# Kernel tuning notes

Measured on AMD Instinct MI355X. Metric: run time of the kernel, lower is better.

Reference implementation:

```python
import jax, jax.numpy as jnp
import numpy as np

DIM = 384
NUM_HEADS = 6
HEAD_DIM = DIM // NUM_HEADS
MLP_HIDDEN = 4 * DIM
SCALE = HEAD_DIM ** -0.5
EPS = 1e-5


def layer_norm(x, w, b):
    mu = jnp.mean(x, axis=-1, keepdims=True)
    var = jnp.mean(jnp.square(x - mu), axis=-1, keepdims=True)
    return (x - mu) * jax.lax.rsqrt(var + EPS) * w + b


def setup_inputs() -> dict:
    key = jax.random.key(0)
    ks = jax.random.split(key, 24)
    d = DIM
    s = 0.02
    inp = {
        'x1': jax.random.normal(ks[0], (16, d, 32, 32), jnp.float32),
        'x2': jax.random.normal(ks[1], (16, d, 32, 32), jnp.float32),
        # per-branch attention-input LayerNorm + kqv projection (no bias)
        'ln_a1_w': jnp.ones((d,), jnp.float32), 'ln_a1_b': jnp.zeros((d,), jnp.float32),
        'kqv1_w': jax.random.normal(ks[2], (d, 3 * d), jnp.float32) * s,
        'ln_a2_w': jnp.ones((d,), jnp.float32), 'ln_a2_b': jnp.zeros((d,), jnp.float32),
        'kqv2_w': jax.random.normal(ks[3], (d, 3 * d), jnp.float32) * s,
        # output projections
        'proj1_w': jax.random.normal(ks[4], (d, d), jnp.float32) * s,
        'proj1_b': jnp.zeros((d,), jnp.float32),
        'proj2_w': jax.random.normal(ks[5], (d, d), jnp.float32) * s,
        'proj2_b': jnp.zeros((d,), jnp.float32),
        # post-attention LayerNorms
        'ln1_w': jnp.ones((d,), jnp.float32), 'ln1_b': jnp.zeros((d,), jnp.float32),
        'ln2_w': jnp.ones((d,), jnp.float32), 'ln2_b': jnp.zeros((d,), jnp.float32),
        # MLPs
        'mlp1_fc1_w': jax.random.normal(ks[6], (d, MLP_HIDDEN), jnp.float32) * s,
        'mlp1_fc1_b': jnp.zeros((MLP_HIDDEN,), jnp.float32),
        'mlp1_fc2_w': jax.random.normal(ks[7], (MLP_HIDDEN, d), jnp.float32) * s,
        'mlp1_fc2_b': jnp.zeros((d,), jnp.float32),
        'mlp2_fc1_w': jax.random.normal(ks[8], (d, MLP_HIDDEN), jnp.float32) * s,
        'mlp2_fc1_b': jnp.zeros((MLP_HIDDEN,), jnp.float32),
        'mlp2_fc2_w': jax.random.normal(ks[9], (MLP_HIDDEN, d), jnp.float32) * s,
        'mlp2_fc2_b': jnp.zeros((d,), jnp.float32),
    }
    return inp


def _kqv_branch(x, ln_w, ln_b, Wkqv):
    # x: [B, C, H, W] -> embedding [B, N, C]; k,q,v: [B, h, N, hd]
    B, C, H, W = x.shape
    N = H * W
    emb = x.reshape(B, C, N).transpose(0, 2, 1)
    xn = layer_norm(emb, ln_w, ln_b)
    kqv = (xn @ Wkqv).reshape(B, N, 3, NUM_HEADS, HEAD_DIM).transpose(2, 0, 3, 1, 4)
    return kqv[0], kqv[1], kqv[2], emb


def _cross_attn(q, k, v):
    # q,k,v: [B, h, N, hd] -> [B, N, C]
    scores = jnp.einsum('bhnd,bhmd->bhnm', q, k) * SCALE
    a = jax.nn.softmax(scores, axis=-1)
    o = jnp.einsum('bhnm,bhmd->bhnd', a, v)
    B, h, N, hd = o.shape
    return o.transpose(0, 2, 1, 3).reshape(B, N, h * hd)


def reference(x1, x2, ln_a1_w, ln_a1_b, kqv1_w, ln_a2_w, ln_a2_b, kqv2_w,
              proj1_w, proj1_b, proj2_w, proj2_b, ln1_w, ln1_b, ln2_w, ln2_b,
              mlp1_fc1_w, mlp1_fc1_b, mlp1_fc2_w, mlp1_fc2_b,
              mlp2_fc1_w, mlp2_fc1_b, mlp2_fc2_w, mlp2_fc2_b):
    B, C, H, W = x1.shape
    k1, q1, v1, emb1 = _kqv_branch(x1, ln_a1_w, ln_a1_b, kqv1_w)
    k2, q2, v2, emb2 = _kqv_branch(x2, ln_a2_w, ln_a2_b, kqv2_w)
    a1 = _cross_attn(q1, k2, v2)   # branch 1 queries attend to branch 2
    a2 = _cross_attn(q2, k1, v1)
    out1 = emb1 + (a1 @ proj1_w + proj1_b)
    h1 = layer_norm(out1, ln1_w, ln1_b)
    out1 = out1 + (jax.nn.gelu(h1 @ mlp1_fc1_w + mlp1_fc1_b, approximate=False) @ mlp1_fc2_w + mlp1_fc2_b)
    out2 = emb2 + (a2 @ proj2_w + proj2_b)
    h2 = layer_norm(out2, ln2_w, ln2_b)
    out2 = out2 + (jax.nn.gelu(h2 @ mlp2_fc1_w + mlp2_fc1_b, approximate=False) @ mlp2_fc2_w + mlp2_fc2_b)
    out1 = out1.transpose(0, 2, 1).reshape(B, C, H, W)
    out2 = out2.transpose(0, 2, 1).reshape(B, C, H, W)
    return (out1, out2)
```

## Files before the change

### kernel.cpp

```cpp
#include <hip/hip_runtime.h>
#include <math.h>

typedef unsigned short u16;
typedef __attribute__((ext_vector_type(8))) short short8;
typedef __attribute__((ext_vector_type(4))) float f32x4;

#define MFMA(a,b,c) __builtin_amdgcn_mfma_f32_16x16x32_bf16(a, b, c, 0, 0, 0)
#define SWZ(row, ch) ((((ch) ^ ((row) & 7)) << 3))
#define EXP2F(x) __builtin_amdgcn_exp2f(x)

__device__ __forceinline__ float b2f(u16 v) {
    union { unsigned int i; float f; } c; c.i = ((unsigned int)v) << 16; return c.f;
}
__device__ __forceinline__ u16 f2b(float f) {
    union { float f; unsigned int i; } c; c.f = f;
    unsigned int u = c.i;
    return (u16)((u + 0x7fffu + ((u >> 16) & 1u)) >> 16);
}
__device__ __forceinline__ u16 f2b_p(float f) {
    union { float f; unsigned int i; } c; c.f = f;
    return (u16)((c.i + 0x8000u) >> 16);
}

struct TWArgs { const float* src[8]; u16* dst[8]; int K[8]; int N[8]; };

__global__ __launch_bounds__(256) void transpose_w(TWArgs a) {
    int wi = blockIdx.z;
    int K = a.K[wi], N = a.N[wi];
    int n0 = blockIdx.x * 32, k0 = blockIdx.y * 32;
    if (n0 >= N || k0 >= K) return;
    __shared__ float t[32][33];
    const float* s = a.src[wi]; u16* d = a.dst[wi];
    int tx = threadIdx.x & 31, ty = threadIdx.x >> 5;
    for (int i = 0; i < 32; i += 8)
        t[ty + i][tx] = s[(size_t)(k0 + ty + i) * N + n0 + tx];
    __syncthreads();
    for (int i = 0; i < 32; i += 8)
        d[(size_t)(n0 + ty + i) * K + k0 + tx] = f2b(t[tx][ty + i]);
}

__global__ __launch_bounds__(256)
void ln_tr(const float* __restrict__ x0, const float* __restrict__ x1,
           const float* __restrict__ w0, const float* __restrict__ bb0,
           const float* __restrict__ w1, const float* __restrict__ bb1,
           u16* __restrict__ xn0, u16* __restrict__ xn1) {
    int br = blockIdx.z;
    const float* x  = br ? x1 : x0;
    const float* wv = br ? w1 : w0;
    const float* bv = br ? bb1 : bb0;
    u16* xn = br ? xn1 : xn0;
    int b = blockIdx.y, n0 = blockIdx.x * 32;
    __shared__ float tile[32][385];
    __shared__ float smu[32], srs[32];
    int tid = threadIdx.x;
    const float* xb = x + (size_t)b * 384 * 1024 + n0;
    for (int idx = tid; idx < 384 * 32; idx += 256) {
        int c = idx >> 5, nn = idx & 31;
        tile[nn][c] = xb[(size_t)c * 1024 + nn];
    }
    __syncthreads();
    {
        int nn = tid >> 3, part = tid & 7;
        float s1 = 0.f, s2 = 0.f;
        for (int c = part * 48; c < part * 48 + 48; ++c) {
            float v = tile[nn][c]; s1 += v; s2 += v * v;
        }
        for (int off = 1; off < 8; off <<= 1) {
            s1 += __shfl_xor(s1, off, 64); s2 += __shfl_xor(s2, off, 64);
        }
        if (part == 0) {
            float mu = s1 * (1.f / 384.f);
            float var = s2 * (1.f / 384.f) - mu * mu;
            smu[nn] = mu; srs[nn] = rsqrtf(fmaxf(var, 0.f) + 1e-5f);
        }
    }
    __syncthreads();
    size_t rowbase = (size_t)b * 1024 + n0;
    for (int idx = tid; idx < 32 * 384; idx += 256) {
        int nn = idx / 384, c = idx - nn * 384;
        float v = tile[nn][c];
        float g = (v - smu[nn]) * srs[nn] * wv[c] + bv[c];
        xn[(rowbase + nn) * 384 + c] = f2b(g);
    }
}

__global__ __launch_bounds__(256)
void ln_rows(const float* __restrict__ i0, const float* __restrict__ i1,
             const float* __restrict__ w0, const float* __restrict__ bb0,
             const float* __restrict__ w1, const float* __restrict__ bb1,
             u16* __restrict__ o0, u16* __restrict__ o1) {
    int br = blockIdx.z;
    const float* in = br ? i1 : i0;
    const float* wv = br ? w1 : w0;
    const float* bv = br ? bb1 : bb0;
    u16* out = br ? o1 : o0;
    int w = threadIdx.x >> 6, l = threadIdx.x & 63;
    size_t row = (size_t)blockIdx.x * 4 + w;
    const float* p = in + row * 384;
    float v[6]; float s1 = 0.f, s2 = 0.f;
    #pragma unroll
    for (int j = 0; j < 6; j++) { v[j] = p[j * 64 + l]; s1 += v[j]; s2 += v[j] * v[j]; }
    for (int off = 1; off < 64; off <<= 1) {
        s1 += __shfl_xor(s1, off, 64); s2 += __shfl_xor(s2, off, 64);
    }
    float mu = s1 * (1.f / 384.f);
    float var = s2 * (1.f / 384.f) - mu * mu;
    float rs = rsqrtf(fmaxf(var, 0.f) + 1e-5f);
    #pragma unroll
    for (int j = 0; j < 6; j++) {
        int c = j * 64 + l;
        out[row * 384 + c] = f2b((v[j] - mu) * rs * wv[c] + bv[c]);
    }
}

template <int EPI>
__global__ __launch_bounds__(256)
void gemm128(const u16* __restrict__ A0, const u16* __restrict__ A1,
             const u16* __restrict__ B0, const u16* __restrict__ B1,
             void* C0v, void* C1v,
             const float* __restrict__ bias0, const float* __restrict__ bias1,
             const void* R0v, const void* R1v,
             int N, int K) {
    const int br = blockIdx.z;
    const u16* A = br ? A1 : A0;
    const u16* B = br ? B1 : B0;
    void* Cv = br ? C1v : C0v;
    const float* bias = br ? bias1 : bias0;
    const void* Rv = br ? R1v : R0v;

    const int n0 = blockIdx.x * 128;
    const int m0 = blockIdx.y * 128;
    const int tid = threadIdx.x;
    const int w = tid >> 6, l = tid & 63;
    const int wm = w >> 1, wn = w & 1;
    const int lr = l & 15, lq = l >> 4;

    __shared__ alignas(16) u16 As[2][128 * 40];
    __shared__ alignas(16) u16 Bs[2][128 * 40];

    f32x4 acc[4][4];
    #pragma unroll
    for (int i = 0; i < 4; i++)
        #pragma unroll
        for (int j = 0; j < 4; j++) acc[i][j] = (f32x4)0.0f;

    const int ar0 = tid >> 2, ac0 = (tid & 3) * 8;
    const int ar1 = ar0 + 64;
    const u16* Ap0 = A + (size_t)(m0 + ar0) * K + ac0;
    const u16* Ap1 = A + (size_t)(m0 + ar1) * K + ac0;
    const u16* Bp0 = B + (size_t)(n0 + ar0) * K + ac0;
    const u16* Bp1 = B + (size_t)(n0 + ar1) * K + ac0;

    const int nk = K >> 5;
    uint4 pa0 = *(const uint4*)Ap0, pa1 = *(const uint4*)Ap1;
    uint4 pb0 = *(const uint4*)Bp0, pb1 = *(const uint4*)Bp1;
    *(uint4*)&As[0][ar0 * 40 + ac0] = pa0;
    *(uint4*)&As[0][ar1 * 40 + ac0] = pa1;
    *(uint4*)&Bs[0][ar0 * 40 + ac0] = pb0;
    *(uint4*)&Bs[0][ar1 * 40 + ac0] = pb1;
    pa0 = *(const uint4*)(Ap0 + 32); pa1 = *(const uint4*)(Ap1 + 32);
    pb0 = *(const uint4*)(Bp0 + 32); pb1 = *(const uint4*)(Bp1 + 32);
    __syncthreads();

    for (int kt = 0; kt < nk; ++kt) {
        const int cur = kt & 1;
        if (kt + 1 < nk) {
            const int nx = cur ^ 1;
            *(uint4*)&As[nx][ar0 * 40 + ac0] = pa0;
            *(uint4*)&As[nx][ar1 * 40 + ac0] = pa1;
            *(uint4*)&Bs[nx][ar0 * 40 + ac0] = pb0;
            *(uint4*)&Bs[nx][ar1 * 40 + ac0] = pb1;
        }
        if (kt + 2 < nk) {
            const int kb = (kt + 2) * 32;
            pa0 = *(const uint4*)(Ap0 + kb); pa1 = *(const uint4*)(Ap1 + kb);
            pb0 = *(const uint4*)(Bp0 + kb); pb1 = *(const uint4*)(Bp1 + kb);
        }
        short8 af[4], bf[4];
        #pragma unroll
        for (int mt = 0; mt < 4; ++mt)
            af[mt] = *(const short8*)&As[cur][(wm * 64 + mt * 16 + lr) * 40 + lq * 8];
        #pragma unroll
        for (int nt = 0; nt < 4; ++nt)
            bf[nt] = *(const short8*)&Bs[cur][(wn * 64 + nt * 16 + lr) * 40 + lq * 8];
        #pragma unroll
        for (int mt = 0; mt < 4; ++mt)
            #pragma unroll
            for (int nt = 0; nt < 4; ++nt)
                acc[mt][nt] = MFMA(af[mt], bf[nt], acc[mt][nt]);
        __syncthreads();
    }

    #pragma unroll
    for (int mt = 0; mt < 4; ++mt)
        #pragma unroll
        for (int nt = 0; nt < 4; ++nt) {
            const int col = n0 + wn * 64 + nt * 16 + lr;
            const int rbase = m0 + wm * 64 + mt * 16 + lq * 4;
            const float bv = (EPI == 0) ? 0.f : bias[col];
            #pragma unroll
            for (int r = 0; r < 4; r++) {
                const int row = rbase + r;
                const size_t idx = (size_t)row * N + col;
                float v = acc[mt][nt][r];
                if (EPI == 0) {
                    if (col < 768) {
                        ((u16*)Cv)[idx] = f2b(col >= 384 ? v * 0.18033688f : v);
                    } else {
                        u16* vtb = (u16*)Rv;
                        vtb[((((size_t)(row >> 10)) * 6 + ((col - 768) >> 6)) * 64
                             + (col & 63)) * 1024 + (row & 1023)] = f2b(v);
                    }
                } else if (EPI == 1) {
                    float xr = ((const float*)Rv)[
                        ((size_t)(row >> 10) * 384 + col) * 1024 + (row & 1023)];
                    ((float*)Cv)[idx] = v + bv + xr;
                } else if (EPI == 2) {
                    v += bv;
                    float g = 0.5f * v * (1.f + erff(v * 0.70710678118f));
                    ((u16*)Cv)[idx] = f2b(g);
                } else {
                    ((float*)Cv)[idx] = v + bv + ((const float*)Rv)[idx];
                }
            }
        }
}

__global__ __launch_bounds__(256)
void attn_k(const u16* __restrict__ kqvA, const u16* __restrict__ kqvB,
            const u16* __restrict__ vtA, const u16* __restrict__ vtB,
            u16* __restrict__ oA, u16* __restrict__ oB) {
    const int bid = blockIdx.x;
    const int g = bid & 7, qb = (bid >> 3) & 7, s = bid >> 6;
    const int grp = s * 8 + g;
    const int ob = grp & 1, h = (grp >> 1) % 6, b = grp / 12;

    const u16* kqvQ  = (ob ? kqvB : kqvA) + (size_t)b * 1024 * 1152;
    const u16* kqvKV = (ob ? kqvA : kqvB) + (size_t)b * 1024 * 1152;
    const u16* vt    = (ob ? vtA : vtB) + ((size_t)b * 6 + h) * 64 * 1024;
    u16* outp = (ob ? oB : oA) + (size_t)b * 1024 * 384;
    const u16* qp = kqvQ + 384 + h * 64;
    const u16* kp = kqvKV + h * 64;

    __shared__ alignas(16) u16 Ks[64 * 64];
    __shared__ alignas(16) u16 Vts[64 * 64];
    __shared__ alignas(16) u16 Ps[4 * 32 * 64];

    const int tid = threadIdx.x, w = tid >> 6, l = tid & 63;
    const int lr = l & 15, lq = l >> 4;
    u16* Psw = Ps + w * 32 * 64;

    short8 qf[2][2];
    #pragma unroll
    for (int a = 0; a < 2; a++)
        #pragma unroll
        for (int ks = 0; ks < 2; ks++)
            qf[a][ks] = *(const short8*)&qp[
                (size_t)(qb * 128 + w * 32 + a * 16 + lr) * 1152 + ks * 32 + lq * 8];

    const int srow = tid >> 3, sch = tid & 7;
    uint4 kpre[2][2], vpre[2][2];
    #pragma unroll
    for (int t = 0; t < 2; t++)
        #pragma unroll
        for (int i = 0; i < 2; i++) {
            int row = srow + i * 32;
            kpre[t][i] = *(const uint4*)&kp[(size_t)(t * 64 + row) * 1152 + sch * 8];
            vpre[t][i] = *(const uint4*)&vt[(size_t)row * 1024 + t * 64 + sch * 8];
        }

    f32x4 oacc[2][4];
    float psum[2][4];
    #pragma unroll
    for (int a = 0; a < 2; a++)
        #pragma unroll
        for (int n = 0; n < 4; n++) oacc[a][n] = (f32x4)0.0f;
    #pragma unroll
    for (int a = 0; a < 2; a++)
        #pragma unroll
        for (int r = 0; r < 4; r++) psum[a][r] = 0.f;

    for (int jt = 0; jt < 16; ++jt) {
        const int slot = jt & 1;
        #pragma unroll
        for (int i = 0; i < 2; i++) {
            int row = srow + i * 32;
            int o = row * 64 + SWZ(row, sch);
            *(uint4*)&Ks[o] = kpre[slot][i];
            *(uint4*)&Vts[o] = vpre[slot][i];
        }
        __syncthreads();
        if (jt + 2 < 16) {
            #pragma unroll
            for (int i = 0; i < 2; i++) {
                int row = srow + i * 32;
                kpre[slot][i] = *(const uint4*)&kp[(size_t)((jt + 2) * 64 + row) * 1152 + sch * 8];
                vpre[slot][i] = *(const uint4*)&vt[(size_t)row * 1024 + (jt + 2) * 64 + sch * 8];
            }
        }

        f32x4 sacc[2][4];
        #pragma unroll
        for (int a = 0; a < 2; a++)
            #pragma unroll
            for (int n = 0; n < 4; n++) sacc[a][n] = (f32x4)0.0f;
        #pragma unroll
        for (int ks = 0; ks < 2; ++ks) {
            short8 bk[4];
            #pragma unroll
            for (int n = 0; n < 4; n++) {
                int row = n * 16 + lr;
                bk[n] = *(const short8*)&Ks[row * 64 + SWZ(row, ks * 4 + lq)];
            }
            #pragma unroll
            for (int a = 0; a < 2; a++)
                #pragma unroll
                for (int n = 0; n < 4; n++) sacc[a][n] = MFMA(qf[a][ks], bk[n], sacc[a][n]);
        }

        #pragma unroll
        for (int a = 0; a < 2; a++)
            #pragma unroll
            for (int r = 0; r < 4; r++) {
                int prow = a * 16 + lq * 4 + r;
                float ps = 0.f;
                #pragma unroll
                for (int n = 0; n < 4; n++) {
                    float p = EXP2F(sacc[a][n][r]);
                    ps += p;
                    Psw[prow * 64 + ((((2 * n + (lr >> 3)) ^ (prow & 7)) << 3) + (lr & 7))] = f2b_p(p);
                }
                psum[a][r] += ps;
            }

        #pragma unroll
        for (int ks = 0; ks < 2; ++ks) {
            short8 ap[2], bv4[4];
            #pragma unroll
            for (int a = 0; a < 2; a++) {
                int row = a * 16 + lr;
                ap[a] = *(const short8*)&Psw[row * 64 + SWZ(row, ks * 4 + lq)];
            }
            #pragma unroll
            for (int n = 0; n < 4; n++) {
                int row = n * 16 + lr;
                bv4[n] = *(const short8*)&Vts[row * 64 + SWZ(row, ks * 4 + lq)];
            }
            #pragma unroll
            for (int a = 0; a < 2; a++)
                #pragma unroll
                for (int n = 0; n < 4; n++) oacc[a][n] = MFMA(ap[a], bv4[n], oacc[a][n]);
        }
        __syncthreads();
    }

    #pragma unroll
    for (int a = 0; a < 2; a++)
        #pragma unroll
        for (int r = 0; r < 4; r++) {
            float sm = psum[a][r];
            sm += __shfl_xor(sm, 1, 64); sm += __shfl_xor(sm, 2, 64);
            sm += __shfl_xor(sm, 4, 64); sm += __shfl_xor(sm, 8, 64);
            psum[a][r] = 1.f / sm;
        }
    #pragma unroll
    for (int a = 0; a < 2; a++)
        #pragma unroll
        for (int n = 0; n < 4; n++)
            #pragma unroll
            for (int r = 0; r < 4; r++) {
                size_t row = (size_t)qb * 128 + w * 32 + a * 16 + lq * 4 + r;
                int col = h * 64 + n * 16 + lr;
                outp[row * 384 + col] = f2b(oacc[a][n][r] * psum[a][r]);
            }
}

__global__ __launch_bounds__(256)
void transpose_out(const float* __restrict__ r0, const float* __restrict__ r1,
                   float* __restrict__ out) {
    int z = blockIdx.z, ob = z >> 4, b = z & 15;
    const float* rp = ob ? r1 : r0;
    int c0 = blockIdx.y * 32, n0 = blockIdx.x * 32;
    __shared__ float t[32][33];
    int tx = threadIdx.x & 31, ty = threadIdx.x >> 5;
    for (int i = 0; i < 32; i += 8)
        t[ty + i][tx] = rp[((size_t)b * 1024 + n0 + ty + i) * 384 + c0 + tx];
    __syncthreads();
    for (int i = 0; i < 32; i += 8)
        out[(size_t)ob * 6291456 + ((size_t)b * 384 + c0 + ty + i) * 1024 + n0 + tx]
            = t[tx][ty + i];
}

extern "C" void kernel_launch(void* const* d_in, const int* in_sizes, int n_in,
                              void* d_out, int out_size, void* d_ws, size_t ws_size,
                              hipStream_t stream) {
    const float* x1      = (const float*)d_in[0];
    const float* x2      = (const float*)d_in[1];
    const float* ln_a1_w = (const float*)d_in[2];
    const float* ln_a1_b = (const float*)d_in[3];
    const float* kqv1_w  = (const float*)d_in[4];
    const float* ln_a2_w = (const float*)d_in[5];
    const float* ln_a2_b = (const float*)d_in[6];
    const float* kqv2_w  = (const float*)d_in[7];
    const float* proj1_w = (const float*)d_in[8];
    const float* proj1_b = (const float*)d_in[9];
    const float* proj2_w = (const float*)d_in[10];
    const float* proj2_b = (const float*)d_in[11];
    const float* ln1_w   = (const float*)d_in[12];
    const float* ln1_b   = (const float*)d_in[13];
    const float* ln2_w   = (const float*)d_in[14];
    const float* ln2_b   = (const float*)d_in[15];
    const float* m1f1w   = (const float*)d_in[16];
    const float* m1f1b   = (const float*)d_in[17];
    const float* m1f2w   = (const float*)d_in[18];
    const float* m1f2b   = (const float*)d_in[19];
    const float* m2f1w   = (const float*)d_in[20];
    const float* m2f1b   = (const float*)d_in[21];
    const float* m2f2w   = (const float*)d_in[22];
    const float* m2f2b   = (const float*)d_in[23];
    (void)in_sizes; (void)n_in; (void)out_size; (void)ws_size;

    const size_t R = 16384;
    char* ws = (char*)d_ws;
    size_t off = 0;
    auto alloc = [&](size_t bytes) -> char* {
        char* p = ws + off;
        off = (off + bytes + 255) & ~(size_t)255;
        return p;
    };
    u16* kqv1t  = (u16*)alloc(1152 * 384 * 2);
    u16* kqv2t  = (u16*)alloc(1152 * 384 * 2);
    u16* proj1t = (u16*)alloc(384 * 384 * 2);
    u16* proj2t = (u16*)alloc(384 * 384 * 2);
    u16* fc11t  = (u16*)alloc(1536 * 384 * 2);
    u16* fc12t  = (u16*)alloc(1536 * 384 * 2);
    u16* fc21t  = (u16*)alloc(384 * 1536 * 2);
    u16* fc22t  = (u16*)alloc(384 * 1536 * 2);
    u16* xn1 = (u16*)alloc(R * 384 * 2);
    u16* xn2 = (u16*)alloc(R * 384 * 2);
    char* regC = alloc(R * 1152 * 2 * 2);
    u16* kqv1 = (u16*)regC;
    u16* kqv2 = (u16*)(regC + R * 1152 * 2);
    float* oa1 = (float*)regC;
    float* oa2 = (float*)(regC + R * 384 * 4);
    u16* hid_b2 = (u16*)(regC + 2 * R * 384 * 4);
    u16* at1 = (u16*)d_out;
    u16* at2 = at1 + R * 384;
    u16* vt1 = at2 + R * 384;
    u16* vt2 = vt1 + (size_t)16 * 6 * 64 * 1024;
    u16* hid_b1 = (u16*)d_out;

    TWArgs tw;
    tw.src[0] = kqv1_w;  tw.dst[0] = kqv1t;  tw.K[0] = 384;  tw.N[0] = 1152;
    tw.src[1] = kqv2_w;  tw.dst[1] = kqv2t;  tw.K[1] = 384;  tw.N[1] = 1152;
    tw.src[2] = proj1_w; tw.dst[2] = proj1t; tw.K[2] = 384;  tw.N[2] = 384;
    tw.src[3] = proj2_w; tw.dst[3] = proj2t; tw.K[3] = 384;  tw.N[3] = 384;
    tw.src[4] = m1f1w;   tw.dst[4] = fc11t;  tw.K[4] = 384;  tw.N[4] = 1536;
    tw.src[5] = m2f1w;   tw.dst[5] = fc12t;  tw.K[5] = 384;  tw.N[5] = 1536;
    tw.src[6] = m1f2w;   tw.dst[6] = fc21t;  tw.K[6] = 1536; tw.N[6] = 384;
    tw.src[7] = m2f2w;   tw.dst[7] = fc22t;  tw.K[7] = 1536; tw.N[7] = 384;
    transpose_w<<<dim3(48, 48, 8), dim3(256), 0, stream>>>(tw);

    ln_tr<<<dim3(32, 16, 2), dim3(256), 0, stream>>>(
        x1, x2, ln_a1_w, ln_a1_b, ln_a2_w, ln_a2_b, xn1, xn2);

    gemm128<0><<<dim3(9, 128, 2), dim3(256), 0, stream>>>(
        xn1, xn2, kqv1t, kqv2t, (void*)kqv1, (void*)kqv2,
        (const float*)nullptr, (const float*)nullptr,
        (const void*)vt1, (const void*)vt2, 1152, 384);

    attn_k<<<dim3(1536), dim3(256), 0, stream>>>(kqv1, kqv2, vt1, vt2, at1, at2);

    gemm128<1><<<dim3(3, 128, 2), dim3(256), 0, stream>>>(
        at1, at2, proj1t, proj2t, (void*)oa1, (void*)oa2,
        proj1_b, proj2_b, (const void*)x1, (const void*)x2, 384, 384);

    ln_rows<<<dim3(4096, 1, 2), dim3(256), 0, stream>>>(
        oa1, oa2, ln1_w, ln1_b, ln2_w, ln2_b, xn1, xn2);

    for (int half = 0; half < 2; ++half) {
        const size_t ro = (size_t)half * 8192;
        gemm128<2><<<dim3(12, 64, 2), dim3(256), 0, stream>>>(
            xn1 + ro * 384, xn2 + ro * 384, fc11t, fc12t,
            (void*)hid_b1, (void*)hid_b2, m1f1b, m2f1b, nullptr, nullptr, 1536, 384);
        gemm128<3><<<dim3(3, 64, 2), dim3(256), 0, stream>>>(
            hid_b1, hid_b2, fc21t, fc22t,
            (void*)(oa1 + ro * 384), (void*)(oa2 + ro * 384),
            m1f2b, m2f2b, (const void*)(oa1 + ro * 384), (const void*)(oa2 + ro * 384),
            384, 1536);
    }

    transpose_out<<<dim3(32, 12, 32), dim3(256), 0, stream>>>(oa1, oa2, (float*)d_out);
}
```

Before: 637.0 us.

## Double-buffer K/V tiles in LDS and raise wave priority around MFMA

The attention kernel now keeps two LDS buffers each for K and V^T. While the current tile is being consumed, the next tile is written from registers into the other buffer, and the global prefetch runs further ahead. This drops one __syncthreads per iteration and moves the LDS stores off the critical path before compute. It also wraps the MFMA sections in s_setprio so those waves are scheduled ahead of others. The cost is twice the LDS for K/V, which may lower occupancy.

```diff
diff --git a/kernel.cpp b/kernel.cpp
--- a/kernel.cpp
+++ b/kernel.cpp
@@ -242,8 +242,8 @@
     const u16* qp = kqvQ + 384 + h * 64;
     const u16* kp = kqvKV + h * 64;
 
-    __shared__ alignas(16) u16 Ks[64 * 64];
-    __shared__ alignas(16) u16 Vts[64 * 64];
+    __shared__ alignas(16) u16 Ks[2][64 * 64];
+    __shared__ alignas(16) u16 Vts[2][64 * 64];
     __shared__ alignas(16) u16 Ps[4 * 32 * 64];
 
     const int tid = threadIdx.x, w = tid >> 6, l = tid & 63;
@@ -269,6 +269,20 @@
             vpre[t][i] = *(const uint4*)&vt[(size_t)row * 1024 + t * 64 + sch * 8];
         }
 
+    #pragma unroll
+    for (int i = 0; i < 2; i++) {
+        int row = srow + i * 32;
+        int o = row * 64 + SWZ(row, sch);
+        *(uint4*)&Ks[0][o] = kpre[0][i];
+        *(uint4*)&Vts[0][o] = vpre[0][i];
+    }
+    #pragma unroll
+    for (int i = 0; i < 2; i++) {
+        int row = srow + i * 32;
+        kpre[0][i] = *(const uint4*)&kp[(size_t)(2 * 64 + row) * 1152 + sch * 8];
+        vpre[0][i] = *(const uint4*)&vt[(size_t)row * 1024 + 2 * 64 + sch * 8];
+    }
+
     f32x4 oacc[2][4];
     float psum[2][4];
     #pragma unroll
@@ -280,22 +294,25 @@
         #pragma unroll
         for (int r = 0; r < 4; r++) psum[a][r] = 0.f;
 
+    __syncthreads();
+
     for (int jt = 0; jt < 16; ++jt) {
-        const int slot = jt & 1;
-        #pragma unroll
-        for (int i = 0; i < 2; i++) {
-            int row = srow + i * 32;
-            int o = row * 64 + SWZ(row, sch);
-            *(uint4*)&Ks[o] = kpre[slot][i];
-            *(uint4*)&Vts[o] = vpre[slot][i];
-        }
-        __syncthreads();
-        if (jt + 2 < 16) {
+        const int cur = jt & 1, nx = cur ^ 1;
+        if (jt + 1 < 16) {
             #pragma unroll
             for (int i = 0; i < 2; i++) {
                 int row = srow + i * 32;
-                kpre[slot][i] = *(const uint4*)&kp[(size_t)((jt + 2) * 64 + row) * 1152 + sch * 8];
-                vpre[slot][i] = *(const uint4*)&vt[(size_t)row * 1024 + (jt + 2) * 64 + sch * 8];
+                int o = row * 64 + SWZ(row, sch);
+                *(uint4*)&Ks[nx][o] = kpre[nx][i];
+                *(uint4*)&Vts[nx][o] = vpre[nx][i];
+            }
+            if (jt + 3 < 16) {
+                #pragma unroll
+                for (int i = 0; i < 2; i++) {
+                    int row = srow + i * 32;
+                    kpre[nx][i] = *(const uint4*)&kp[(size_t)((jt + 3) * 64 + row) * 1152 + sch * 8];
+                    vpre[nx][i] = *(const uint4*)&vt[(size_t)row * 1024 + (jt + 3) * 64 + sch * 8];
+                }
             }
         }
 
@@ -304,19 +321,21 @@
         for (int a = 0; a < 2; a++)
             #pragma unroll
             for (int n = 0; n < 4; n++) sacc[a][n] = (f32x4)0.0f;
+        __builtin_amdgcn_s_setprio(1);
         #pragma unroll
         for (int ks = 0; ks < 2; ++ks) {
             short8 bk[4];
             #pragma unroll
             for (int n = 0; n < 4; n++) {
                 int row = n * 16 + lr;
-                bk[n] = *(const short8*)&Ks[row * 64 + SWZ(row, ks * 4 + lq)];
+                bk[n] = *(const short8*)&Ks[cur][row * 64 + SWZ(row, ks * 4 + lq)];
             }
             #pragma unroll
             for (int a = 0; a < 2; a++)
                 #pragma unroll
                 for (int n = 0; n < 4; n++) sacc[a][n] = MFMA(qf[a][ks], bk[n], sacc[a][n]);
         }
+        __builtin_amdgcn_s_setprio(0);
 
         #pragma unroll
         for (int a = 0; a < 2; a++)
@@ -333,6 +352,7 @@
                 psum[a][r] += ps;
             }
 
+        __builtin_amdgcn_s_setprio(1);
         #pragma unroll
         for (int ks = 0; ks < 2; ++ks) {
             short8 ap[2], bv4[4];
@@ -344,13 +364,14 @@
             #pragma unroll
             for (int n = 0; n < 4; n++) {
                 int row = n * 16 + lr;
-                bv4[n] = *(const short8*)&Vts[row * 64 + SWZ(row, ks * 4 + lq)];
+                bv4[n] = *(const short8*)&Vts[cur][row * 64 + SWZ(row, ks * 4 + lq)];
             }
             #pragma unroll
             for (int a = 0; a < 2; a++)
                 #pragma unroll
                 for (int n = 0; n < 4; n++) oacc[a][n] = MFMA(ap[a], bv4[n], oacc[a][n]);
         }
+        __builtin_amdgcn_s_setprio(0);
         __syncthreads();
     }
 
```

New measurement: 638.2 us. No clear change (+0.2%).
